# Optimization experiments

Hardware: AMD Instinct MI355X
Metric: run time of the kernel (lower is better)

## Reference

```python
import jax, jax.numpy as jnp
import numpy as np

D_DIM = 128
K_DIM = 32


def setup_inputs() -> dict:
    key = jax.random.key(0)
    k1, k2, k3 = jax.random.split(key, 3)
    B, H, W = 8, 64, 64
    std1 = 1.0 / (K_DIM * D_DIM) ** 0.5
    std2 = 1.0 / K_DIM ** 0.5
    X = jax.random.normal(k1, (B, D_DIM, H, W), dtype=jnp.float32)
    codewords = jax.random.uniform(k2, (K_DIM, D_DIM), dtype=jnp.float32, minval=-std1, maxval=std1)
    scale = jax.random.uniform(k3, (K_DIM,), dtype=jnp.float32, minval=-std2, maxval=std2)
    return {"X": X, "codewords": codewords, "scale": scale}


def reference(X, codewords, scale):
    # X: [B, D, H, W] -> descriptors [B, N, D]
    B, D, H, W = X.shape
    Xf = X.reshape(B, D, H * W).transpose(0, 2, 1)  # [B, N, D]
    # Squared distance ||x - c||^2 expanded: avoids materializing [B,N,K,D]
    x_sq = jnp.sum(Xf * Xf, axis=-1, keepdims=True)          # [B, N, 1]
    c_sq = jnp.sum(codewords * codewords, axis=-1)           # [K]
    cross = jnp.einsum('bnd,kd->bnk', Xf, codewords)         # [B, N, K]
    dist2 = x_sq - 2.0 * cross + c_sq                        # [B, N, K]
    # NOTE: faithful to source -- softmax over scale * dist^2 (no negation)
    A = jax.nn.softmax(dist2 * scale, axis=-1)               # [B, N, K]
    # E[b,k,d] = sum_n A[b,n,k] * (x[b,n,d] - c[k,d])
    E = jnp.einsum('bnk,bnd->bkd', A, Xf) - jnp.sum(A, axis=1)[..., None] * codewords
    return E  # [B, K, D]
```

## Files before the change

### kernel.cpp

```cpp
#include <hip/hip_runtime.h>

#define D_DIM 128
#define K_DIM 32
#define NPIX  4096
#define TPB   64

typedef __bf16 bf16x8 __attribute__((ext_vector_type(8)));
typedef unsigned short u16x8 __attribute__((ext_vector_type(8)));
typedef float f32x4 __attribute__((ext_vector_type(4)));

__device__ __forceinline__ unsigned short f2bf(float f) {
    union { float f; unsigned u; } v; v.f = f;
    unsigned r = v.u + 0x7FFFu + ((v.u >> 16) & 1u);
    return (unsigned short)(r >> 16);
}
__device__ __forceinline__ unsigned pack2(float lo, float hi) {
    return (unsigned)f2bf(lo) | ((unsigned)f2bf(hi) << 16);
}
__device__ __forceinline__ float bf2f(unsigned short u) {
    union { unsigned u; float f; } v; v.u = ((unsigned)u) << 16;
    return v.f;
}
__device__ __forceinline__ bf16x8 ldfrag(const unsigned short* p) {
    union { u16x8 s; bf16x8 b; } u;
    u.s = *(const u16x8*)p;
    return u.b;
}

__global__ __launch_bounds__(256) void zero_out_kernel(float* __restrict__ out) {
    int i = blockIdx.x * 256 + threadIdx.x;
    ((float4*)out)[i] = make_float4(0.f, 0.f, 0.f, 0.f);
}

#define XDN_LD 72
#define XND_LD 136
#define CW_LD  136
#define SA_LD  72

__global__ __launch_bounds__(256, 2) void enc_kernel(
    const float* __restrict__ X,
    const float* __restrict__ cw,
    const float* __restrict__ scale,
    float* __restrict__ out)
{
    __shared__ __align__(16) unsigned short sXdn[D_DIM * XDN_LD];
    __shared__ __align__(16) unsigned short sXnd[TPB * XND_LD];
    __shared__ __align__(16) unsigned short sCW[K_DIM * CW_LD];
    __shared__ __align__(16) unsigned short sA[K_DIM * SA_LD];
    __shared__ float sXsqP[16 * 65];
    __shared__ float sXsq[TPB];
    __shared__ float sSum[K_DIM];
    __shared__ float sSc[K_DIM];
    __shared__ float sCS[K_DIM];

    const int ltid = threadIdx.x;
    const int b    = blockIdx.x >> 6;
    const int n0   = (blockIdx.x & 63) * TPB;
    const int lane = ltid & 63;
    const int w    = ltid >> 6;
    const int l15  = lane & 15;
    const int quad = lane >> 4;

    if (ltid < K_DIM) {
        const float4* cr = (const float4*)(cw + ltid * D_DIM);
        float cs = 0.f;
        #pragma unroll 8
        for (int q = 0; q < 32; ++q) {
            float4 c4 = cr[q];
            cs = fmaf(c4.x, c4.x, fmaf(c4.y, c4.y, fmaf(c4.z, c4.z, fmaf(c4.w, c4.w, cs))));
        }
        float s = scale[ltid];
        sSc[ltid] = s;
        sCS[ltid] = cs * s;
        sSum[ltid] = 0.f;
    }

    {
        const int r  = ltid >> 3;
        const int q8 = ltid & 7;
        #pragma unroll
        for (int i = 0; i < 4; ++i) {
            const int col = 16 * q8 + 4 * i;
            float4 c4 = *(const float4*)(cw + r * D_DIM + col);
            *(uint2*)&sCW[r * CW_LD + col] =
                make_uint2(pack2(c4.x, c4.y), pack2(c4.z, c4.w));
        }
    }

    {
        const int c  = ltid & 15;
        const int rp = ltid >> 4;
        float px[4] = {0.f, 0.f, 0.f, 0.f};
        const float* xb = X + (size_t)b * D_DIM * NPIX + n0;
        #pragma unroll
        for (int p = 0; p < 4; ++p) {
            const int R  = rp + 16 * p;
            const int d0 = 2 * R;
            float4 f0 = *(const float4*)(xb + (size_t)d0 * NPIX + 4 * c);
            float4 f1 = *(const float4*)(xb + (size_t)(d0 + 1) * NPIX + 4 * c);
            px[0] = fmaf(f0.x, f0.x, fmaf(f1.x, f1.x, px[0]));
            px[1] = fmaf(f0.y, f0.y, fmaf(f1.y, f1.y, px[1]));
            px[2] = fmaf(f0.z, f0.z, fmaf(f1.z, f1.z, px[2]));
            px[3] = fmaf(f0.w, f0.w, fmaf(f1.w, f1.w, px[3]));
            *(uint2*)&sXdn[d0 * XDN_LD + 4 * c] =
                make_uint2(pack2(f0.x, f0.y), pack2(f0.z, f0.w));
            *(uint2*)&sXdn[(d0 + 1) * XDN_LD + 4 * c] =
                make_uint2(pack2(f1.x, f1.y), pack2(f1.z, f1.w));
            *(unsigned*)&sXnd[(4 * c + 0) * XND_LD + d0] = pack2(f0.x, f1.x);
            *(unsigned*)&sXnd[(4 * c + 1) * XND_LD + d0] = pack2(f0.y, f1.y);
            *(unsigned*)&sXnd[(4 * c + 2) * XND_LD + d0] = pack2(f0.z, f1.z);
            *(unsigned*)&sXnd[(4 * c + 3) * XND_LD + d0] = pack2(f0.w, f1.w);
        }
        #pragma unroll
        for (int j = 0; j < 4; ++j) sXsqP[rp * 65 + 4 * c + j] = px[j];
    }
    __syncthreads();

    if (ltid < TPB) {
        float s = 0.f;
        #pragma unroll
        for (int rp = 0; rp < 16; ++rp) s += sXsqP[rp * 65 + ltid];
        sXsq[ltid] = s;
    }

    f32x4 accA[2] = {{0.f, 0.f, 0.f, 0.f}, {0.f, 0.f, 0.f, 0.f}};
    {
        const int prow = (16 * w + l15) * XND_LD;
        #pragma unroll
        for (int ks = 0; ks < 4; ++ks) {
            const int off = 8 * quad + 32 * ks;
            bf16x8 bfrag = ldfrag(&sXnd[prow + off]);
            bf16x8 a0 = ldfrag(&sCW[l15 * CW_LD + off]);
            bf16x8 a1 = ldfrag(&sCW[(l15 + 16) * CW_LD + off]);
            accA[0] = __builtin_amdgcn_mfma_f32_16x16x32_bf16(a0, bfrag, accA[0], 0, 0, 0);
            accA[1] = __builtin_amdgcn_mfma_f32_16x16x32_bf16(a1, bfrag, accA[1], 0, 0, 0);
        }
    }
    __syncthreads();

    {
        const float xsq = sXsq[16 * w + l15];
        float e8[8];
        float psum = 0.f;
        #pragma unroll
        for (int mt = 0; mt < 2; ++mt)
            #pragma unroll
            for (int reg = 0; reg < 4; ++reg) {
                const int k = 16 * mt + 4 * quad + reg;
                float cross = accA[mt][reg];
                float l = fmaf(sSc[k], fmaf(-2.f, cross, xsq), sCS[k]);
                float e = __expf(l);
                e8[4 * mt + reg] = e;
                psum += e;
            }
        psum += __shfl_xor(psum, 16);
        psum += __shfl_xor(psum, 32);
        const float inv = 1.f / psum;
        float r8[8];
        #pragma unroll
        for (int i = 0; i < 8; ++i) {
            float a = e8[i] * inv;
            e8[i] = a;
            r8[i] = a;
        }
        #pragma unroll
        for (int mt = 0; mt < 2; ++mt)
            #pragma unroll
            for (int reg = 0; reg < 4; ++reg) {
                const int k = 16 * mt + 4 * quad + reg;
                sA[k * SA_LD + 16 * w + l15] = f2bf(e8[4 * mt + reg]);
            }
        #pragma unroll
        for (int i = 0; i < 8; ++i) {
            r8[i] += __shfl_xor(r8[i], 1);
            r8[i] += __shfl_xor(r8[i], 2);
            r8[i] += __shfl_xor(r8[i], 4);
            r8[i] += __shfl_xor(r8[i], 8);
        }
        if (l15 == 0) {
            #pragma unroll
            for (int mt = 0; mt < 2; ++mt)
                #pragma unroll
                for (int reg = 0; reg < 4; ++reg)
                    atomicAdd(&sSum[16 * mt + 4 * quad + reg], r8[4 * mt + reg]);
        }
    }
    __syncthreads();

    f32x4 accE[2][2] = {{{0.f,0.f,0.f,0.f},{0.f,0.f,0.f,0.f}},
                        {{0.f,0.f,0.f,0.f},{0.f,0.f,0.f,0.f}}};
    {
        const int drow0 = (l15 + 16 * (2 * w + 0)) * XDN_LD;
        const int drow1 = (l15 + 16 * (2 * w + 1)) * XDN_LD;
        #pragma unroll
        for (int ks = 0; ks < 2; ++ks) {
            const int off = 8 * quad + 32 * ks;
            bf16x8 a0 = ldfrag(&sA[l15 * SA_LD + off]);
            bf16x8 a1 = ldfrag(&sA[(l15 + 16) * SA_LD + off]);
            bf16x8 b0 = ldfrag(&sXdn[drow0 + off]);
            bf16x8 b1 = ldfrag(&sXdn[drow1 + off]);
            accE[0][0] = __builtin_amdgcn_mfma_f32_16x16x32_bf16(a0, b0, accE[0][0], 0, 0, 0);
            accE[0][1] = __builtin_amdgcn_mfma_f32_16x16x32_bf16(a0, b1, accE[0][1], 0, 0, 0);
            accE[1][0] = __builtin_amdgcn_mfma_f32_16x16x32_bf16(a1, b0, accE[1][0], 0, 0, 0);
            accE[1][1] = __builtin_amdgcn_mfma_f32_16x16x32_bf16(a1, b1, accE[1][1], 0, 0, 0);
        }
    }

    {
        float* outb = out + (size_t)b * (K_DIM * D_DIM);
        float sk[8];
        #pragma unroll
        for (int mt = 0; mt < 2; ++mt)
            #pragma unroll
            for (int reg = 0; reg < 4; ++reg)
                sk[4 * mt + reg] = sSum[16 * mt + 4 * quad + reg];
        #pragma unroll
        for (int mt = 0; mt < 2; ++mt) {
            #pragma unroll
            for (int rr = 0; rr < 4; ++rr) {
                const int reg = (rr + blockIdx.x) & 3;
                const int k = 16 * mt + 4 * quad + reg;
                #pragma unroll
                for (int dt = 0; dt < 2; ++dt) {
                    const int d = 16 * (2 * w + dt) + l15;
                    float cwv = bf2f(sCW[k * CW_LD + d]);
                    float v = fmaf(-sk[4 * mt + reg], cwv, accE[mt][dt][reg]);
                    atomicAdd(outb + k * D_DIM + d, v);
                }
            }
        }
    }
}

extern "C" void kernel_launch(void* const* d_in, const int* in_sizes, int n_in,
                              void* d_out, int out_size, void* d_ws, size_t ws_size,
                              hipStream_t stream) {
    const float* X  = (const float*)d_in[0];
    const float* cw = (const float*)d_in[1];
    const float* sc = (const float*)d_in[2];
    float* out = (float*)d_out;
    (void)in_sizes; (void)n_in; (void)d_ws; (void)ws_size; (void)out_size;

    hipLaunchKernelGGL(zero_out_kernel, dim3(32), dim3(256), 0, stream, out);
    hipLaunchKernelGGL(enc_kernel, dim3(512), dim3(256), 0, stream, X, cw, sc, out);
}
```

Before: 76.20 us.

## Double pixel tile per block and drop transposed X copy from LDS

Each block now covers 128 pixels with 512 threads (256 blocks instead of 512), which halves the number of global atomic adds into the output. The D-major shared copy of X is removed. The second MFMA stage instead re-reads X from global memory and converts it to bf16 fragments in registers, relying on cache hits to save LDS space and store traffic. The codeword load is also widened to 16-byte stores. The trade-offs are fewer blocks to fill the GPU, a second global read of X, and more threads per block competing for occupancy.

```diff
diff --git a/kernel.cpp b/kernel.cpp
--- a/kernel.cpp
+++ b/kernel.cpp
@@ -3,7 +3,7 @@
 #define D_DIM 128
 #define K_DIM 32
 #define NPIX  4096
-#define TPB   64
+#define TPB   128
 
 typedef __bf16 bf16x8 __attribute__((ext_vector_type(8)));
 typedef unsigned short u16x8 __attribute__((ext_vector_type(8)));
@@ -26,36 +26,40 @@
     u.s = *(const u16x8*)p;
     return u.b;
 }
+__device__ __forceinline__ bf16x8 pack8(float4 a, float4 b) {
+    union { unsigned d[4]; bf16x8 v; } u;
+    u.d[0] = pack2(a.x, a.y); u.d[1] = pack2(a.z, a.w);
+    u.d[2] = pack2(b.x, b.y); u.d[3] = pack2(b.z, b.w);
+    return u.v;
+}
 
 __global__ __launch_bounds__(256) void zero_out_kernel(float* __restrict__ out) {
     int i = blockIdx.x * 256 + threadIdx.x;
     ((float4*)out)[i] = make_float4(0.f, 0.f, 0.f, 0.f);
 }
 
-#define XDN_LD 72
 #define XND_LD 136
 #define CW_LD  136
-#define SA_LD  72
-
-__global__ __launch_bounds__(256, 2) void enc_kernel(
+#define SA_LD  136
+
+__global__ __launch_bounds__(512, 2) void enc_kernel(
     const float* __restrict__ X,
     const float* __restrict__ cw,
     const float* __restrict__ scale,
     float* __restrict__ out)
 {
-    __shared__ __align__(16) unsigned short sXdn[D_DIM * XDN_LD];
     __shared__ __align__(16) unsigned short sXnd[TPB * XND_LD];
     __shared__ __align__(16) unsigned short sCW[K_DIM * CW_LD];
     __shared__ __align__(16) unsigned short sA[K_DIM * SA_LD];
-    __shared__ float sXsqP[16 * 65];
+    __shared__ float sXsqP[16 * 129];
     __shared__ float sXsq[TPB];
     __shared__ float sSum[K_DIM];
     __shared__ float sSc[K_DIM];
     __shared__ float sCS[K_DIM];
 
     const int ltid = threadIdx.x;
-    const int b    = blockIdx.x >> 6;
-    const int n0   = (blockIdx.x & 63) * TPB;
+    const int b    = blockIdx.x >> 5;
+    const int n0   = (blockIdx.x & 31) * TPB;
     const int lane = ltid & 63;
     const int w    = ltid >> 6;
     const int l15  = lane & 15;
@@ -76,50 +80,50 @@
     }
 
     {
-        const int r  = ltid >> 3;
-        const int q8 = ltid & 7;
-        #pragma unroll
-        for (int i = 0; i < 4; ++i) {
-            const int col = 16 * q8 + 4 * i;
-            float4 c4 = *(const float4*)(cw + r * D_DIM + col);
-            *(uint2*)&sCW[r * CW_LD + col] =
-                make_uint2(pack2(c4.x, c4.y), pack2(c4.z, c4.w));
-        }
-    }
-
-    {
-        const int c  = ltid & 15;
-        const int rp = ltid >> 4;
+        const int r  = ltid >> 4;
+        const int q8 = ltid & 15;
+        float4 c0 = *(const float4*)(cw + r * D_DIM + 8 * q8);
+        float4 c1 = *(const float4*)(cw + r * D_DIM + 8 * q8 + 4);
+        uint4 pk;
+        pk.x = pack2(c0.x, c0.y); pk.y = pack2(c0.z, c0.w);
+        pk.z = pack2(c1.x, c1.y); pk.w = pack2(c1.z, c1.w);
+        *(uint4*)&sCW[r * CW_LD + 8 * q8] = pk;
+    }
+
+    {
+        const int c   = ltid & 15;
+        const int rp  = (ltid >> 4) & 3;
+        const int ph  = ltid >> 6;
+        const int pxh = (ph & 1) * 64;
+        const int dbl = (ph >> 1) * 16;
         float px[4] = {0.f, 0.f, 0.f, 0.f};
-        const float* xb = X + (size_t)b * D_DIM * NPIX + n0;
+        const float* xb = X + (size_t)b * D_DIM * NPIX + n0 + pxh;
         #pragma unroll
         for (int p = 0; p < 4; ++p) {
-            const int R  = rp + 16 * p;
-            const int d0 = 2 * R;
+            const int pair = rp + 4 * p + dbl;
+            const int d0   = 2 * pair;
             float4 f0 = *(const float4*)(xb + (size_t)d0 * NPIX + 4 * c);
             float4 f1 = *(const float4*)(xb + (size_t)(d0 + 1) * NPIX + 4 * c);
             px[0] = fmaf(f0.x, f0.x, fmaf(f1.x, f1.x, px[0]));
             px[1] = fmaf(f0.y, f0.y, fmaf(f1.y, f1.y, px[1]));
             px[2] = fmaf(f0.z, f0.z, fmaf(f1.z, f1.z, px[2]));
             px[3] = fmaf(f0.w, f0.w, fmaf(f1.w, f1.w, px[3]));
-            *(uint2*)&sXdn[d0 * XDN_LD + 4 * c] =
-                make_uint2(pack2(f0.x, f0.y), pack2(f0.z, f0.w));
-            *(uint2*)&sXdn[(d0 + 1) * XDN_LD + 4 * c] =
-                make_uint2(pack2(f1.x, f1.y), pack2(f1.z, f1.w));
-            *(unsigned*)&sXnd[(4 * c + 0) * XND_LD + d0] = pack2(f0.x, f1.x);
-            *(unsigned*)&sXnd[(4 * c + 1) * XND_LD + d0] = pack2(f0.y, f1.y);
-            *(unsigned*)&sXnd[(4 * c + 2) * XND_LD + d0] = pack2(f0.z, f1.z);
-            *(unsigned*)&sXnd[(4 * c + 3) * XND_LD + d0] = pack2(f0.w, f1.w);
-        }
-        #pragma unroll
-        for (int j = 0; j < 4; ++j) sXsqP[rp * 65 + 4 * c + j] = px[j];
+            const int pix = pxh + 4 * c;
+            *(unsigned*)&sXnd[(pix + 0) * XND_LD + d0] = pack2(f0.x, f1.x);
+            *(unsigned*)&sXnd[(pix + 1) * XND_LD + d0] = pack2(f0.y, f1.y);
+            *(unsigned*)&sXnd[(pix + 2) * XND_LD + d0] = pack2(f0.z, f1.z);
+            *(unsigned*)&sXnd[(pix + 3) * XND_LD + d0] = pack2(f0.w, f1.w);
+        }
+        const int row = rp + 4 * (ph >> 1);
+        #pragma unroll
+        for (int j = 0; j < 4; ++j) sXsqP[row * 129 + pxh + 4 * c + j] = px[j];
     }
     __syncthreads();
 
     if (ltid < TPB) {
         float s = 0.f;
         #pragma unroll
-        for (int rp = 0; rp < 16; ++rp) s += sXsqP[rp * 65 + ltid];
+        for (int r = 0; r < 16; ++r) s += sXsqP[r * 129 + ltid];
         sXsq[ltid] = s;
     }
 
@@ -147,8 +151,7 @@
             #pragma unroll
             for (int reg = 0; reg < 4; ++reg) {
                 const int k = 16 * mt + 4 * quad + reg;
-                float cross = accA[mt][reg];
-                float l = fmaf(sSc[k], fmaf(-2.f, cross, xsq), sCS[k]);
+                float l = fmaf(sSc[k], fmaf(-2.f, accA[mt][reg], xsq), sCS[k]);
                 float e = __expf(l);
                 e8[4 * mt + reg] = e;
                 psum += e;
@@ -159,9 +162,8 @@
         float r8[8];
         #pragma unroll
         for (int i = 0; i < 8; ++i) {
-            float a = e8[i] * inv;
-            e8[i] = a;
-            r8[i] = a;
+            e8[i] *= inv;
+            r8[i] = e8[i];
         }
         #pragma unroll
         for (int mt = 0; mt < 2; ++mt)
@@ -187,46 +189,41 @@
     }
     __syncthreads();
 
-    f32x4 accE[2][2] = {{{0.f,0.f,0.f,0.f},{0.f,0.f,0.f,0.f}},
-                        {{0.f,0.f,0.f,0.f},{0.f,0.f,0.f,0.f}}};
-    {
-        const int drow0 = (l15 + 16 * (2 * w + 0)) * XDN_LD;
-        const int drow1 = (l15 + 16 * (2 * w + 1)) * XDN_LD;
-        #pragma unroll
-        for (int ks = 0; ks < 2; ++ks) {
+    f32x4 accE[2] = {{0.f, 0.f, 0.f, 0.f}, {0.f, 0.f, 0.f, 0.f}};
+    {
+        const int d = 16 * w + l15;
+        const float* xrow = X + ((size_t)b * D_DIM + d) * NPIX + n0;
+        float4 g[4][2];
+        #pragma unroll
+        for (int ks = 0; ks < 4; ++ks) {
+            const float* p = xrow + 8 * quad + 32 * ks;
+            g[ks][0] = *(const float4*)p;
+            g[ks][1] = *(const float4*)(p + 4);
+        }
+        #pragma unroll
+        for (int ks = 0; ks < 4; ++ks) {
             const int off = 8 * quad + 32 * ks;
+            bf16x8 bfrag = pack8(g[ks][0], g[ks][1]);
             bf16x8 a0 = ldfrag(&sA[l15 * SA_LD + off]);
             bf16x8 a1 = ldfrag(&sA[(l15 + 16) * SA_LD + off]);
-            bf16x8 b0 = ldfrag(&sXdn[drow0 + off]);
-            bf16x8 b1 = ldfrag(&sXdn[drow1 + off]);
-            accE[0][0] = __builtin_amdgcn_mfma_f32_16x16x32_bf16(a0, b0, accE[0][0], 0, 0, 0);
-            accE[0][1] = __builtin_amdgcn_mfma_f32_16x16x32_bf16(a0, b1, accE[0][1], 0, 0, 0);
-            accE[1][0] = __builtin_amdgcn_mfma_f32_16x16x32_bf16(a1, b0, accE[1][0], 0, 0, 0);
-            accE[1][1] = __builtin_amdgcn_mfma_f32_16x16x32_bf16(a1, b1, accE[1][1], 0, 0, 0);
+            accE[0] = __builtin_amdgcn_mfma_f32_16x16x32_bf16(a0, bfrag, accE[0], 0, 0, 0);
+            accE[1] = __builtin_amdgcn_mfma_f32_16x16x32_bf16(a1, bfrag, accE[1], 0, 0, 0);
         }
     }
 
     {
         float* outb = out + (size_t)b * (K_DIM * D_DIM);
-        float sk[8];
-        #pragma unroll
-        for (int mt = 0; mt < 2; ++mt)
-            #pragma unroll
-            for (int reg = 0; reg < 4; ++reg)
-                sk[4 * mt + reg] = sSum[16 * mt + 4 * quad + reg];
+        const int d = 16 * w + l15;
         #pragma unroll
         for (int mt = 0; mt < 2; ++mt) {
             #pragma unroll
             for (int rr = 0; rr < 4; ++rr) {
                 const int reg = (rr + blockIdx.x) & 3;
                 const int k = 16 * mt + 4 * quad + reg;
-                #pragma unroll
-                for (int dt = 0; dt < 2; ++dt) {
-                    const int d = 16 * (2 * w + dt) + l15;
-                    float cwv = bf2f(sCW[k * CW_LD + d]);
-                    float v = fmaf(-sk[4 * mt + reg], cwv, accE[mt][dt][reg]);
-                    atomicAdd(outb + k * D_DIM + d, v);
-                }
+                float sk  = sSum[k];
+                float cwv = bf2f(sCW[k * CW_LD + d]);
+                float v = fmaf(-sk, cwv, accE[mt][reg]);
+                atomicAdd(outb + k * D_DIM + d, v);
             }
         }
     }
@@ -242,5 +239,5 @@
     (void)in_sizes; (void)n_in; (void)d_ws; (void)ws_size; (void)out_size;
 
     hipLaunchKernelGGL(zero_out_kernel, dim3(32), dim3(256), 0, stream, out);
-    hipLaunchKernelGGL(enc_kernel, dim3(512), dim3(256), 0, stream, X, cw, sc, out);
-}
+    hipLaunchKernelGGL(enc_kernel, dim3(256), dim3(512), 0, stream, X, cw, sc, out);
+}
```

After: 73.09 us. 4.1% less time.
